# Optimization experiments

Measured on AMD Instinct MI355X. Metric: run time of the kernel, lower is better.

## Reference

```python
import jax, jax.numpy as jnp
import numpy as np
from jax import lax

WINDOW_SIZE = 11
GAUSSIAN_SIGMA = 1.5
C1 = (0.01 * 255.0) ** 2
C2 = (0.03 * 255.0) ** 2


def _gaussian_window(ws: int, sigma: float) -> np.ndarray:
    # matches cv2.getGaussianKernel(ws, sigma) outer-product window
    ax = np.arange(ws, dtype=np.float64) - (ws - 1) / 2.0
    g = np.exp(-(ax ** 2) / (2.0 * sigma ** 2))
    g = g / g.sum()
    return np.outer(g, g)  # [ws, ws], sums to 1


def _depthwise_conv(x, kernel):
    # x: [B, C, H, W]; kernel: [ws, ws] shared across channels (groups=C)
    c = x.shape[1]
    k = jnp.broadcast_to(kernel.astype(x.dtype)[None, None], (c, 1, kernel.shape[0], kernel.shape[1]))
    return lax.conv_general_dilated(
        x, k, window_strides=(1, 1), padding='VALID',
        dimension_numbers=('NCHW', 'OIHW', 'NCHW'),
        feature_group_count=c)


def setup_inputs() -> dict:
    key = jax.random.key(0)
    k1, k2 = jax.random.split(key)
    shape = (16, 3, 512, 512)
    raw_tensor = jax.random.uniform(k1, shape, dtype=jnp.float32)
    dst_tensor = jax.random.uniform(k2, shape, dtype=jnp.float32)
    return {"raw_tensor": raw_tensor, "dst_tensor": dst_tensor}


def reference(raw_tensor, dst_tensor):
    window = jnp.asarray(_gaussian_window(WINDOW_SIZE, GAUSSIAN_SIGMA), dtype=raw_tensor.dtype)
    raw = raw_tensor * 255.0
    dst = dst_tensor * 255.0

    raw_mean = _depthwise_conv(raw, window)
    dst_mean = _depthwise_conv(dst, window)
    raw_mean_sq = raw_mean ** 2
    dst_mean_sq = dst_mean ** 2
    raw_dst_mean = raw_mean * dst_mean

    raw_var = _depthwise_conv(raw * raw, window) - raw_mean_sq
    dst_var = _depthwise_conv(dst * dst, window) - dst_mean_sq
    raw_dst_cov = _depthwise_conv(raw * dst, window) - raw_dst_mean

    numer = (2.0 * raw_dst_mean + C1) * (2.0 * raw_dst_cov + C2)
    denom = (raw_mean_sq + dst_mean_sq + C1) * (raw_var + dst_var + C2)
    ssim_map = numer / denom  # [B, C, H-ws+1, W-ws+1]
    return jnp.mean(ssim_map, axis=(1, 2, 3))  # [B]
```

## Files before the change

### kernel.cpp

```cpp
#include <hip/hip_runtime.h>
#include <math.h>


#define WSZ 11
#define IMG 512
#define OSZ 502
#define NT  256
#define CH_OUT 32
#define NCHUNK 16
#define NS 12
#define LA 6

struct WinArg { float w[WSZ]; };

typedef float f2 __attribute__((ext_vector_type(2)));
typedef float f4v __attribute__((ext_vector_type(4)));

typedef const __attribute__((address_space(1))) unsigned int* gp_t;
typedef __attribute__((address_space(3))) unsigned int* sp_t;

#define C1V 1.0e-4f
#define C2V 9.0e-4f

__device__ __forceinline__ void pkfma(f2& acc, f2 a, f2 b) {
    acc = __builtin_elementwise_fma(a, b, acc);
}

__global__ __launch_bounds__(NT, 2) void ssim_ilp2(
    const float* __restrict__ rawp, const float* __restrict__ dstp,
    float* __restrict__ out, WinArg wa, float inv_n)
{
    __shared__ f4v srow[3648];
    __shared__ float wred[NT / 64];

    const int tid  = threadIdx.x;
    const int lane = tid & 63;
    const int wave = tid >> 6;
    const int chunk = blockIdx.x;
    const int img   = blockIdx.y;

    const int o0    = chunk * CH_OUT;
    const int olim  = min(o0 + CH_OUT, OSZ);
    const int rlast = min(o0 + CH_OUT + WSZ - 2, IMG - 1);
    const int NR    = rlast - o0 + 1;

    const bool w3     = (wave == 3);
    const int  nch    = w3 ? 4 : 5;
    const int  slotf4 = w3 ? 64 : 80;
    f4v* region = srow + wave * 960;
    const int  rl     = (w3 && lane > 58) ? 58 : lane;
    const bool active = !(w3 && lane > 58);

    const size_t ibase = (size_t)img * (size_t)(IMG * IMG);
    const float* lane_base = ((lane & 1) ? dstp : rawp) + ibase
                           + (size_t)(wave * 128 + (lane >> 1));

    f2 wv[WSZ];
#pragma unroll
    for (int j = 0; j < WSZ; ++j) { wv[j].x = wa.w[j]; wv[j].y = wa.w[j]; }

#define STAGE(ROW, SLOT)                                                       \
    {                                                                          \
        const float* _s = lane_base + (size_t)(ROW) * IMG;                     \
        float* _d = (float*)(region + (SLOT) * slotf4);                        \
        _Pragma("unroll")                                                      \
        for (int _c = 0; _c < 5; ++_c) {                                       \
            if (_c < nch)                                                      \
                __builtin_amdgcn_global_load_lds(                              \
                    (gp_t)(const void*)(_s + 32 * _c),                         \
                    (sp_t)(void*)(_d + 64 * _c), 4, 0, 0);                     \
        }                                                                      \
    }

#define HPASS(QQ, KS)                                                          \
    {                                                                          \
        f2 s12a = {0.f, 0.f}, s34a = {0.f, 0.f};                               \
        f2 s12b = {0.f, 0.f}, s34b = {0.f, 0.f};                               \
        _Pragma("unroll")                                                      \
        for (int e = 0; e < 12; ++e) {                                         \
            const f2 rd = (e & 1) ? QQ[e >> 1].zw : QQ[e >> 1].xy;             \
            const f2 rr2 = rd * rd;                                            \
            f2 sp;                                                             \
            sp.x = rr2.x + rr2.y;                                              \
            sp.y = rd.x * rd.y;                                                \
            if (e < 11) { pkfma(s12a, wv[e], rd); pkfma(s34a, wv[e], sp); }    \
            if (e >= 1) { pkfma(s12b, wv[e-1], rd); pkfma(s34b, wv[e-1], sp); }\
        }                                                                      \
        hs12[KS][0] = s12a; hs34[KS][0] = s34a;                                \
        hs12[KS][1] = s12b; hs34[KS][1] = s34b;                                \
    }

#define VPASS(KOFF)                                                            \
    {                                                                          \
        f2 m12a = {0.f, 0.f}, m34a = {0.f, 0.f};                               \
        f2 m12b = {0.f, 0.f}, m34b = {0.f, 0.f};                               \
        _Pragma("unroll")                                                      \
        for (int i = 0; i < WSZ; ++i) {                                        \
            const int s = ((KOFF) + i) % NS;                                   \
            pkfma(m12a, wv[i], hs12[s][0]);                                    \
            pkfma(m34a, wv[i], hs34[s][0]);                                    \
            pkfma(m12b, wv[i], hs12[s][1]);                                    \
            pkfma(m34b, wv[i], hs34[s][1]);                                    \
        }                                                                      \
        {                                                                      \
            const float m1 = m12a.x, m2 = m12a.y;                              \
            const float m3 = m34a.x, m4 = m34a.y;                              \
            const float q1 = m1 * m1, q2 = m2 * m2, mm = m1 * m2;              \
            const float num = (2.f * mm + C1V) * (2.f * (m4 - mm) + C2V);      \
            const float den = (q1 + q2 + C1V) * (((m3 - q1) - q2) + C2V);      \
            acc += num * __builtin_amdgcn_rcpf(den);                           \
        }                                                                      \
        {                                                                      \
            const float m1 = m12b.x, m2 = m12b.y;                              \
            const float m3 = m34b.x, m4 = m34b.y;                              \
            const float q1 = m1 * m1, q2 = m2 * m2, mm = m1 * m2;              \
            const float num = (2.f * mm + C1V) * (2.f * (m4 - mm) + C2V);      \
            const float den = (q1 + q2 + C1V) * (((m3 - q1) - q2) + C2V);      \
            acc += num * __builtin_amdgcn_rcpf(den);                           \
        }                                                                      \
    }

    f2 hs12[NS][2];
    f2 hs34[NS][2];
    float acc = 0.0f;

#pragma unroll
    for (int r = 0; r < LA; ++r) STAGE(o0 + r, r)

#pragma unroll 1
    for (int rr = 0; rr < NR; rr += NS) {
#pragma unroll
        for (int S = 0; S < NS / 2; ++S) {
            const int klin = rr + 2 * S;
            if (klin < NR) {
                {
                    int ra = klin + 6; if (ra > NR - 1) ra = NR - 1;
                    int rb = klin + 7; if (rb > NR - 1) rb = NR - 1;
                    STAGE(o0 + ra, (2 * S + 6) % NS)
                    STAGE(o0 + rb, (2 * S + 7) % NS)
                }
                if (!w3) asm volatile("s_waitcnt vmcnt(30)" ::: "memory");
                else     asm volatile("s_waitcnt vmcnt(24)" ::: "memory");

                f4v q0[6], q1[6];
                {
                    const f4v* rp0 = region + ((2 * S)     % NS) * slotf4 + rl;
                    const f4v* rp1 = region + ((2 * S + 1) % NS) * slotf4 + rl;
#pragma unroll
                    for (int j = 0; j < 6; ++j) q0[j] = rp0[j];
#pragma unroll
                    for (int j = 0; j < 6; ++j) q1[j] = rp1[j];
                }

                HPASS(q0, (2 * S) % NS)
                if (klin >= WSZ - 1 && (o0 + klin - (WSZ - 1)) < olim && active)
                    VPASS((2 * S + 2) % NS)

                HPASS(q1, (2 * S + 1) % NS)
                if (klin + 1 >= WSZ - 1 && (o0 + klin + 1 - (WSZ - 1)) < olim && active)
                    VPASS((2 * S + 3) % NS)
            }
        }
    }
#undef STAGE
#undef HPASS
#undef VPASS

#pragma unroll
    for (int off = 32; off > 0; off >>= 1) acc += __shfl_down(acc, off, 64);
    if (lane == 0) wred[wave] = acc;
    __syncthreads();
    if (tid == 0) {
        const float tot = (wred[0] + wred[1]) + (wred[2] + wred[3]);
        atomicAdd(out + img / 3, tot * inv_n);
    }
}

extern "C" void kernel_launch(void* const* d_in, const int* in_sizes, int n_in,
                              void* d_out, int out_size, void* d_ws, size_t ws_size,
                              hipStream_t stream) {
    const float* raw = (const float*)d_in[0];
    const float* dst = (const float*)d_in[1];
    float* out = (float*)d_out;

    hipMemsetAsync(out, 0, (size_t)out_size * sizeof(float), stream);

    WinArg wa;
    double g[WSZ], s = 0.0;
    for (int i = 0; i < WSZ; ++i) {
        double ax = (double)i - (double)(WSZ - 1) / 2.0;
        g[i] = exp(-(ax * ax) / (2.0 * 1.5 * 1.5));
        s += g[i];
    }
    for (int i = 0; i < WSZ; ++i) wa.w[i] = (float)(g[i] / s);

    const float inv_n = (float)(1.0 / (3.0 * (double)OSZ * (double)OSZ));

    dim3 grid(NCHUNK, 48);
    ssim_ilp2<<<grid, NT, 0, stream>>>(raw, dst, out, wa, inv_n);
}
```

Baseline: 62.30 us.

## Process one row per step with deferred vertical pass and higher occupancy

Restructures the main loop from two rows per step to one row per step, staging one row ahead and running the vertical pass for the previous row before the horizontal pass of the current one. A final vertical pass after the loop picks up the last output row. Launch bounds are raised to three blocks per SIMD so fewer live registers allow more concurrent waves to hide load latency. The trade-off is less instruction-level parallelism per step and a tighter register budget that may cause spills.

```diff
diff --git a/kernel.cpp b/kernel.cpp
--- a/kernel.cpp
+++ b/kernel.cpp
@@ -26,7 +26,7 @@
     acc = __builtin_elementwise_fma(a, b, acc);
 }
 
-__global__ __launch_bounds__(NT, 2) void ssim_ilp2(
+__global__ __launch_bounds__(NT, 3) void ssim_vs(
     const float* __restrict__ rawp, const float* __restrict__ dstp,
     float* __restrict__ out, WinArg wa, float inv_n)
 {
@@ -72,24 +72,6 @@
         }                                                                      \
     }
 
-#define HPASS(QQ, KS)                                                          \
-    {                                                                          \
-        f2 s12a = {0.f, 0.f}, s34a = {0.f, 0.f};                               \
-        f2 s12b = {0.f, 0.f}, s34b = {0.f, 0.f};                               \
-        _Pragma("unroll")                                                      \
-        for (int e = 0; e < 12; ++e) {                                         \
-            const f2 rd = (e & 1) ? QQ[e >> 1].zw : QQ[e >> 1].xy;             \
-            const f2 rr2 = rd * rd;                                            \
-            f2 sp;                                                             \
-            sp.x = rr2.x + rr2.y;                                              \
-            sp.y = rd.x * rd.y;                                                \
-            if (e < 11) { pkfma(s12a, wv[e], rd); pkfma(s34a, wv[e], sp); }    \
-            if (e >= 1) { pkfma(s12b, wv[e-1], rd); pkfma(s34b, wv[e-1], sp); }\
-        }                                                                      \
-        hs12[KS][0] = s12a; hs34[KS][0] = s34a;                                \
-        hs12[KS][1] = s12b; hs34[KS][1] = s34b;                                \
-    }
-
 #define VPASS(KOFF)                                                            \
     {                                                                          \
         f2 m12a = {0.f, 0.f}, m34a = {0.f, 0.f};                               \
@@ -130,40 +112,54 @@
 #pragma unroll 1
     for (int rr = 0; rr < NR; rr += NS) {
 #pragma unroll
-        for (int S = 0; S < NS / 2; ++S) {
-            const int klin = rr + 2 * S;
+        for (int k = 0; k < NS; ++k) {
+            const int klin = rr + k;
             if (klin < NR) {
                 {
-                    int ra = klin + 6; if (ra > NR - 1) ra = NR - 1;
-                    int rb = klin + 7; if (rb > NR - 1) rb = NR - 1;
-                    STAGE(o0 + ra, (2 * S + 6) % NS)
-                    STAGE(o0 + rb, (2 * S + 7) % NS)
+                    int rs = klin + LA; if (rs > NR - 1) rs = NR - 1;
+                    STAGE(o0 + rs, (k + LA) % NS)
                 }
-                if (!w3) asm volatile("s_waitcnt vmcnt(30)" ::: "memory");
-                else     asm volatile("s_waitcnt vmcnt(24)" ::: "memory");
+                asm volatile("s_waitcnt vmcnt(24)" ::: "memory");
 
-                f4v q0[6], q1[6];
+                f4v q[6];
                 {
-                    const f4v* rp0 = region + ((2 * S)     % NS) * slotf4 + rl;
-                    const f4v* rp1 = region + ((2 * S + 1) % NS) * slotf4 + rl;
+                    const f4v* rp = region + k * slotf4 + rl;
 #pragma unroll
-                    for (int j = 0; j < 6; ++j) q0[j] = rp0[j];
-#pragma unroll
-                    for (int j = 0; j < 6; ++j) q1[j] = rp1[j];
+                    for (int j = 0; j < 6; ++j) q[j] = rp[j];
                 }
 
-                HPASS(q0, (2 * S) % NS)
-                if (klin >= WSZ - 1 && (o0 + klin - (WSZ - 1)) < olim && active)
-                    VPASS((2 * S + 2) % NS)
+                if (klin >= WSZ && (o0 + klin - WSZ) < olim && active)
+                    VPASS((k + 1) % NS)
 
-                HPASS(q1, (2 * S + 1) % NS)
-                if (klin + 1 >= WSZ - 1 && (o0 + klin + 1 - (WSZ - 1)) < olim && active)
-                    VPASS((2 * S + 3) % NS)
+                f2 s12a = {0.f, 0.f}, s34a = {0.f, 0.f};
+                f2 s12b = {0.f, 0.f}, s34b = {0.f, 0.f};
+#pragma unroll
+                for (int e = 0; e < 12; ++e) {
+                    const f2 rd = (e & 1) ? q[e >> 1].zw : q[e >> 1].xy;
+                    const f2 rr2 = rd * rd;
+                    f2 sp;
+                    sp.x = rr2.x + rr2.y;
+                    sp.y = rd.x * rd.y;
+                    if (e < 11) {
+                        pkfma(s12a, wv[e], rd);
+                        pkfma(s34a, wv[e], sp);
+                    }
+                    if (e >= 1) {
+                        pkfma(s12b, wv[e - 1], rd);
+                        pkfma(s34b, wv[e - 1], sp);
+                    }
+                }
+                hs12[k][0] = s12a; hs34[k][0] = s34a;
+                hs12[k][1] = s12b; hs34[k][1] = s34b;
             }
         }
     }
+
+    if (active) {
+        if (NR == 42) { VPASS(7) }
+        else          { VPASS(9) }
+    }
 #undef STAGE
-#undef HPASS
 #undef VPASS
 
 #pragma unroll
@@ -197,5 +193,5 @@
     const float inv_n = (float)(1.0 / (3.0 * (double)OSZ * (double)OSZ));
 
     dim3 grid(NCHUNK, 48);
-    ssim_ilp2<<<grid, NT, 0, stream>>>(raw, dst, out, wa, inv_n);
+    ssim_vs<<<grid, NT, 0, stream>>>(raw, dst, out, wa, inv_n);
 }
```

After: 66.34 us. 1.06x slower.
